# Performance work log

Hardware: AMD Instinct MI355X
Metric: run time of the kernel (lower is better)

## Reference

```python
import jax, jax.numpy as jnp
import numpy as np

V, D, H = 32000, 512, 512
B, T, MAX_LEN = 32, 128, 48


def setup_inputs() -> dict:
    key = jax.random.key(0)
    ks = jax.random.split(key, 12)
    s = 0.02  # xavier-ish scale
    return {
        "inputs": jax.random.randint(ks[0], (B, 1), 0, V),
        "context": jax.random.normal(ks[1], (B, 1, H), dtype=jnp.float32),
        "max_len": MAX_LEN,
        "encoder_outputs": jax.random.normal(ks[2], (B, T, H), dtype=jnp.float32),
        "emb": jax.random.normal(ks[3], (V, D), dtype=jnp.float32) * s,
        "gru_Wih": jax.random.normal(ks[4], (3 * H, D + H), dtype=jnp.float32) * s,
        "gru_Whh": jax.random.normal(ks[5], (3 * H, H), dtype=jnp.float32) * s,
        "gru_bih": jax.random.normal(ks[6], (3 * H,), dtype=jnp.float32) * s,
        "gru_bhh": jax.random.normal(ks[7], (3 * H,), dtype=jnp.float32) * s,
        "lin_W": jax.random.normal(ks[8], (V, 2 * H), dtype=jnp.float32) * s,
        "lin_b": jax.random.normal(ks[9], (V,), dtype=jnp.float32) * s,
        "attn_W": jax.random.normal(ks[10], (H, H), dtype=jnp.float32) * s,
        "attn_b": jax.random.normal(ks[11], (H,), dtype=jnp.float32) * s,
    }


def reference(inputs, context, max_len, encoder_outputs, emb, gru_Wih, gru_Whh,
              gru_bih, gru_bhh, lin_W, lin_b, attn_W, attn_b):
    Bsz, Tlen, Hdim = encoder_outputs.shape
    ctx0 = context[:, 0, :]          # B,H  (last encoder hidden)
    e0 = emb[inputs[:, 0]]           # B,D  (start symbol embedding)
    h0 = jnp.zeros((Bsz, Hdim), dtype=context.dtype)
    # attn linear on encoder outputs is loop-invariant -> hoist
    energies = jnp.einsum('bth,gh->btg', encoder_outputs, attn_W) + attn_b  # B,T,H

    def gru_step(x, h):
        gi = x @ gru_Wih.T + gru_bih
        gh = h @ gru_Whh.T + gru_bhh
        ir, iz, inn = jnp.split(gi, 3, axis=-1)
        hr, hz, hn = jnp.split(gh, 3, axis=-1)
        r = jax.nn.sigmoid(ir + hr)
        z = jax.nn.sigmoid(iz + hz)
        n = jnp.tanh(inn + r * hn)
        return (1.0 - z) * n + z * h

    def step(carry, _):
        h, ctx, e = carry
        h = gru_step(jnp.concatenate([e, ctx], axis=-1), h)
        score = jnp.concatenate([h, ctx], axis=-1) @ lin_W.T + lin_b  # B,V
        logp = jax.nn.log_softmax(score, axis=-1)
        e_next = emb[jnp.argmax(logp, axis=-1)]                       # greedy feedback
        alpha = jax.nn.softmax(jnp.einsum('bth,bh->bt', energies, h), axis=-1)
        ctx_next = jnp.einsum('bt,bth->bh', alpha, encoder_outputs)
        return (h, ctx_next, e_next), logp

    _, logps = jax.lax.scan(step, (h0, ctx0, e0), None, length=max_len)
    # logps: (max_len, B, V) -> cat along dim1 then view => (B*max_len, V)
    return jnp.transpose(logps, (1, 0, 2)).reshape(Bsz * max_len, -1)
```

## Files before the change

### kernel.cpp

```cpp
#include <hip/hip_runtime.h>
#include <hip/hip_bf16.h>

#define V  32000
#define D  512
#define H  512
#define B  32
#define T  128
#define L  48
#define KLIN 1024
#define KGRU 1536

typedef __attribute__((ext_vector_type(8))) short bf16x8;
typedef __attribute__((ext_vector_type(4))) float f32x4;

__device__ __forceinline__ void split1(float f, unsigned short* hi, unsigned short* lo) {
    unsigned u  = __float_as_uint(f);
    unsigned uh = u + (0x7FFFu + ((u >> 16) & 1u));
    unsigned short hs = (unsigned short)(uh >> 16);
    float hf = __uint_as_float(((unsigned)hs) << 16);
    float l  = f - hf;
    unsigned ul = __float_as_uint(l);
    ul += 0x7FFFu + ((ul >> 16) & 1u);
    *hi = hs;
    *lo = (unsigned short)(ul >> 16);
}

__device__ __forceinline__ void split8(const float* __restrict__ p, bf16x8& hi, bf16x8& lo) {
    float4 w0 = reinterpret_cast<const float4*>(p)[0];
    float4 w1 = reinterpret_cast<const float4*>(p)[1];
    float w[8] = {w0.x, w0.y, w0.z, w0.w, w1.x, w1.y, w1.z, w1.w};
    #pragma unroll
    for (int i = 0; i < 8; ++i) {
        unsigned u  = __float_as_uint(w[i]);
        unsigned uh = u + (0x7FFFu + ((u >> 16) & 1u));
        unsigned short hs = (unsigned short)(uh >> 16);
        float hf = __uint_as_float(((unsigned)hs) << 16);
        float l  = w[i] - hf;
        unsigned ul = __float_as_uint(l);
        ul += 0x7FFFu + ((ul >> 16) & 1u);
        hi[i] = (short)hs;
        lo[i] = (short)(ul >> 16);
    }
}

__global__ void presplit_lin(const float* __restrict__ src,
                             unsigned short* __restrict__ hi, unsigned short* __restrict__ lo)
{
    long i = (long)blockIdx.x * 256 + threadIdx.x;
    if (i >= (long)V * KLIN / 8) return;
    bf16x8 h8, l8;
    split8(src + i * 8, h8, l8);
    *(bf16x8*)(hi + i * 8) = h8;
    *(bf16x8*)(lo + i * 8) = l8;
}

__global__ void presplit_gru(const float* __restrict__ Wih, const float* __restrict__ Whh,
                             unsigned short* __restrict__ hi, unsigned short* __restrict__ lo)
{
    int i = blockIdx.x * 256 + threadIdx.x;
    if (i >= 1536 * 192) return;
    int col = i / 192, k = (i % 192) * 8;
    const float* src = (k < 1024) ? (Wih + (size_t)col * 1024 + k)
                                  : (Whh + (size_t)col * 512 + (k - 1024));
    bf16x8 h8, l8;
    split8(src, h8, l8);
    *(bf16x8*)(hi + (size_t)col * KGRU + k) = h8;
    *(bf16x8*)(lo + (size_t)col * KGRU + k) = l8;
}

__global__ void init_state(const int* __restrict__ inputs, const float* __restrict__ context,
                           const float* __restrict__ emb, float* __restrict__ h_t,
                           unsigned short* __restrict__ Xghi, unsigned short* __restrict__ Xglo,
                           unsigned short* __restrict__ Xlhi, unsigned short* __restrict__ Xllo)
{
    int idx = blockIdx.x * 256 + threadIdx.x;
    int b = idx >> 9, j = idx & 511;
    int tok = inputs[b];
    float e = emb[(size_t)tok * D + j];
    split1(e, &Xghi[b * KGRU + j], &Xglo[b * KGRU + j]);
    float c = context[b * H + j];
    split1(c, &Xghi[b * KGRU + 512 + j], &Xglo[b * KGRU + 512 + j]);
    split1(c, &Xlhi[b * KLIN + 512 + j], &Xllo[b * KLIN + 512 + j]);
    Xghi[b * KGRU + 1024 + j] = 0;
    Xglo[b * KGRU + 1024 + j] = 0;
    h_t[j * 32 + b] = 0.f;
}

__global__ void __launch_bounds__(256) energies_gemm(
    const float* __restrict__ enc, const float* __restrict__ attnW,
    const float* __restrict__ attnb, float* __restrict__ energies)
{
    int wave = threadIdx.x >> 6, lane = threadIdx.x & 63;
    int col = blockIdx.y * 64 + wave * 16 + (lane & 15);
    int kg  = (lane >> 4) * 8;
    int arow0 = blockIdx.x * 32 + (lane & 15);
    f32x4 acc0 = {0.f,0.f,0.f,0.f}, acc1 = {0.f,0.f,0.f,0.f};
    for (int k0 = 0; k0 < 512; k0 += 32) {
        bf16x8 bh, bl;  split8(attnW + (size_t)col * 512 + k0 + kg, bh, bl);
        bf16x8 a0h, a0l; split8(enc + (size_t)arow0 * 512 + k0 + kg, a0h, a0l);
        bf16x8 a1h, a1l; split8(enc + (size_t)(arow0 + 16) * 512 + k0 + kg, a1h, a1l);
        acc0 = __builtin_amdgcn_mfma_f32_16x16x32_bf16(a0h, bh, acc0, 0, 0, 0);
        acc1 = __builtin_amdgcn_mfma_f32_16x16x32_bf16(a1h, bh, acc1, 0, 0, 0);
        acc0 = __builtin_amdgcn_mfma_f32_16x16x32_bf16(a0l, bh, acc0, 0, 0, 0);
        acc1 = __builtin_amdgcn_mfma_f32_16x16x32_bf16(a1l, bh, acc1, 0, 0, 0);
        acc0 = __builtin_amdgcn_mfma_f32_16x16x32_bf16(a0h, bl, acc0, 0, 0, 0);
        acc1 = __builtin_amdgcn_mfma_f32_16x16x32_bf16(a1h, bl, acc1, 0, 0, 0);
    }
    float bias = attnb[col];
    int r0 = (lane >> 4) * 4;
    #pragma unroll
    for (int i = 0; i < 4; ++i) {
        int row = blockIdx.x * 32 + r0 + i;
        energies[(size_t)row * 512 + col]        = acc0[i] + bias;
        energies[(size_t)(row + 16) * 512 + col] = acc1[i] + bias;
    }
}

__global__ void __launch_bounds__(384) gru_fused(
    const unsigned short* __restrict__ Ghi, const unsigned short* __restrict__ Glo,
    const unsigned short* __restrict__ Xghi_r, const unsigned short* __restrict__ Xglo_r,
    unsigned short* __restrict__ Xghi_w, unsigned short* __restrict__ Xglo_w,
    unsigned short* __restrict__ Xlhi_w, unsigned short* __restrict__ Xllo_w,
    const float* __restrict__ bih, const float* __restrict__ bhh,
    float* __restrict__ h_t)
{
    __shared__ float AI[3][32][16], AH[3][32][16];
    __shared__ float R[32][16], Z[32][16];
    int w = threadIdx.x >> 6, lane = threadIdx.x & 63;
    int g = (w < 3) ? w : w - 3;
    int half = (w >= 3) ? 1 : 0;
    int c = lane & 15, grp = lane >> 4, kg = grp * 8;
    int j = blockIdx.x * 16 + c;
    int gcol = g * 512 + j;
    const unsigned short* wh = Ghi + (size_t)gcol * KGRU;
    const unsigned short* wl = Glo + (size_t)gcol * KGRU;
    const unsigned short* xh = Xghi_r + (size_t)c * KGRU;
    const unsigned short* xl = Xglo_r + (size_t)c * KGRU;
    f32x4 aI0 = {0.f,0.f,0.f,0.f}, aI1 = {0.f,0.f,0.f,0.f};
    f32x4 aH0 = {0.f,0.f,0.f,0.f}, aH1 = {0.f,0.f,0.f,0.f};
    for (int k0 = half * 512; k0 < half * 512 + 512; k0 += 32) {
        bf16x8 bh = *(const bf16x8*)(wh + k0 + kg);
        bf16x8 bl = *(const bf16x8*)(wl + k0 + kg);
        bf16x8 a0h = *(const bf16x8*)(xh + k0 + kg);
        bf16x8 a0l = *(const bf16x8*)(xl + k0 + kg);
        bf16x8 a1h = *(const bf16x8*)(xh + 16 * KGRU + k0 + kg);
        bf16x8 a1l = *(const bf16x8*)(xl + 16 * KGRU + k0 + kg);
        aI0 = __builtin_amdgcn_mfma_f32_16x16x32_bf16(a0h, bh, aI0, 0, 0, 0);
        aI1 = __builtin_amdgcn_mfma_f32_16x16x32_bf16(a1h, bh, aI1, 0, 0, 0);
        aI0 = __builtin_amdgcn_mfma_f32_16x16x32_bf16(a0l, bh, aI0, 0, 0, 0);
        aI1 = __builtin_amdgcn_mfma_f32_16x16x32_bf16(a1l, bh, aI1, 0, 0, 0);
        aI0 = __builtin_amdgcn_mfma_f32_16x16x32_bf16(a0h, bl, aI0, 0, 0, 0);
        aI1 = __builtin_amdgcn_mfma_f32_16x16x32_bf16(a1h, bl, aI1, 0, 0, 0);
    }
    for (int k0 = 1024 + half * 256; k0 < 1024 + half * 256 + 256; k0 += 32) {
        bf16x8 bh = *(const bf16x8*)(wh + k0 + kg);
        bf16x8 bl = *(const bf16x8*)(wl + k0 + kg);
        bf16x8 a0h = *(const bf16x8*)(xh + k0 + kg);
        bf16x8 a0l = *(const bf16x8*)(xl + k0 + kg);
        bf16x8 a1h = *(const bf16x8*)(xh + 16 * KGRU + k0 + kg);
        bf16x8 a1l = *(const bf16x8*)(xl + 16 * KGRU + k0 + kg);
        aH0 = __builtin_amdgcn_mfma_f32_16x16x32_bf16(a0h, bh, aH0, 0, 0, 0);
        aH1 = __builtin_amdgcn_mfma_f32_16x16x32_bf16(a1h, bh, aH1, 0, 0, 0);
        aH0 = __builtin_amdgcn_mfma_f32_16x16x32_bf16(a0l, bh, aH0, 0, 0, 0);
        aH1 = __builtin_amdgcn_mfma_f32_16x16x32_bf16(a1l, bh, aH1, 0, 0, 0);
        aH0 = __builtin_amdgcn_mfma_f32_16x16x32_bf16(a0h, bl, aH0, 0, 0, 0);
        aH1 = __builtin_amdgcn_mfma_f32_16x16x32_bf16(a1h, bl, aH1, 0, 0, 0);
    }
    if (w >= 3) {
        #pragma unroll
        for (int i = 0; i < 4; ++i) {
            AI[g][grp * 4 + i][c] = aI0[i];  AI[g][grp * 4 + i + 16][c] = aI1[i];
            AH[g][grp * 4 + i][c] = aH0[i];  AH[g][grp * 4 + i + 16][c] = aH1[i];
        }
    }
    __syncthreads();
    float gi[8], gh[8];
    if (w < 3) {
        float bi = bih[gcol], bhv = bhh[gcol];
        #pragma unroll
        for (int i = 0; i < 4; ++i) {
            gi[i]     = aI0[i] + AI[g][grp * 4 + i][c]      + bi;
            gi[i + 4] = aI1[i] + AI[g][grp * 4 + i + 16][c] + bi;
            gh[i]     = aH0[i] + AH[g][grp * 4 + i][c]      + bhv;
            gh[i + 4] = aH1[i] + AH[g][grp * 4 + i + 16][c] + bhv;
        }
        if (w == 0) {
            #pragma unroll
            for (int i = 0; i < 8; ++i) {
                int b = (i < 4) ? grp * 4 + i : grp * 4 + (i - 4) + 16;
                R[b][c] = 1.f / (1.f + expf(-(gi[i] + gh[i])));
            }
        } else if (w == 1) {
            #pragma unroll
            for (int i = 0; i < 8; ++i) {
                int b = (i < 4) ? grp * 4 + i : grp * 4 + (i - 4) + 16;
                Z[b][c] = 1.f / (1.f + expf(-(gi[i] + gh[i])));
            }
        }
    }
    __syncthreads();
    if (w == 2) {
        float4 h0 = *(const float4*)(h_t + (size_t)j * 32 + grp * 4);
        float4 h1 = *(const float4*)(h_t + (size_t)j * 32 + grp * 4 + 16);
        float hold[8] = {h0.x, h0.y, h0.z, h0.w, h1.x, h1.y, h1.z, h1.w};
        float hn[8];
        #pragma unroll
        for (int i = 0; i < 8; ++i) {
            int b = (i < 4) ? grp * 4 + i : grp * 4 + (i - 4) + 16;
            float n = tanhf(gi[i] + R[b][c] * gh[i]);
            float z = Z[b][c];
            hn[i] = (1.f - z) * n + z * hold[i];
        }
        *(float4*)(h_t + (size_t)j * 32 + grp * 4)      = make_float4(hn[0], hn[1], hn[2], hn[3]);
        *(float4*)(h_t + (size_t)j * 32 + grp * 4 + 16) = make_float4(hn[4], hn[5], hn[6], hn[7]);
        #pragma unroll
        for (int i = 0; i < 8; ++i) {
            int b = (i < 4) ? grp * 4 + i : grp * 4 + (i - 4) + 16;
            split1(hn[i], &Xlhi_w[(size_t)b * KLIN + j], &Xllo_w[(size_t)b * KLIN + j]);
            split1(hn[i], &Xghi_w[(size_t)b * KGRU + 1024 + j], &Xglo_w[(size_t)b * KGRU + 1024 + j]);
        }
    }
}

template<bool PS>
__global__ void __launch_bounds__(256) score_attn(
    const float* __restrict__ linW,
    const unsigned short* __restrict__ Whi, const unsigned short* __restrict__ Wlo,
    const float* __restrict__ linb,
    const unsigned short* __restrict__ Xlhi_r, const unsigned short* __restrict__ Xllo_r,
    unsigned short* __restrict__ Xlhi_w, unsigned short* __restrict__ Xllo_w,
    unsigned short* __restrict__ Xghi_w, unsigned short* __restrict__ Xglo_w,
    const float* __restrict__ h_t, const float* __restrict__ energies,
    const float* __restrict__ enc,
    float* __restrict__ out, float* __restrict__ Pm, float* __restrict__ Ps,
    int* __restrict__ Pa, int t)
{
    __shared__ float Lm[4][32], Ls[4][32];
    __shared__ int   La[4][32];
    __shared__ float hrow[512], aw[128], red[256];
    int tid = threadIdx.x;
    if (blockIdx.x < 500) {
        int wave = tid >> 6, lane = tid & 63;
        int c = lane & 15, grp = lane >> 4, kg = grp * 8;
        int col = blockIdx.x * 64 + wave * 16 + c;
        const unsigned short* x0h = Xlhi_r + (size_t)c * KLIN + kg;
        const unsigned short* x0l = Xllo_r + (size_t)c * KLIN + kg;
        f32x4 acc0 = {0.f,0.f,0.f,0.f}, acc1 = {0.f,0.f,0.f,0.f};
        #pragma unroll 2
        for (int k0 = 0; k0 < 1024; k0 += 32) {
            bf16x8 bh, bl;
            if (PS) {
                bh = *(const bf16x8*)(Whi + (size_t)col * 1024 + k0 + kg);
                bl = *(const bf16x8*)(Wlo + (size_t)col * 1024 + k0 + kg);
            } else {
                split8(linW + (size_t)col * 1024 + k0 + kg, bh, bl);
            }
            bf16x8 a0h = *(const bf16x8*)(x0h + k0);
            bf16x8 a0l = *(const bf16x8*)(x0l + k0);
            bf16x8 a1h = *(const bf16x8*)(x0h + 16 * KLIN + k0);
            bf16x8 a1l = *(const bf16x8*)(x0l + 16 * KLIN + k0);
            acc0 = __builtin_amdgcn_mfma_f32_16x16x32_bf16(a0h, bh, acc0, 0, 0, 0);
            acc1 = __builtin_amdgcn_mfma_f32_16x16x32_bf16(a1h, bh, acc1, 0, 0, 0);
            acc0 = __builtin_amdgcn_mfma_f32_16x16x32_bf16(a0l, bh, acc0, 0, 0, 0);
            acc1 = __builtin_amdgcn_mfma_f32_16x16x32_bf16(a1l, bh, acc1, 0, 0, 0);
            acc0 = __builtin_amdgcn_mfma_f32_16x16x32_bf16(a0h, bl, acc0, 0, 0, 0);
            acc1 = __builtin_amdgcn_mfma_f32_16x16x32_bf16(a1h, bl, acc1, 0, 0, 0);
        }
        float bias = linb[col];
        float v[8];
        int r0 = grp * 4;
        #pragma unroll
        for (int i = 0; i < 4; ++i) {
            v[i]     = acc0[i] + bias;
            v[i + 4] = acc1[i] + bias;
            out[(size_t)((r0 + i) * L + t) * V + col]      = v[i];
            out[(size_t)((r0 + i + 16) * L + t) * V + col] = v[i + 4];
        }
        #pragma unroll
        for (int i = 0; i < 8; ++i) {
            float m = v[i]; int mc = col;
            #pragma unroll
            for (int d = 1; d < 16; d <<= 1) {
                float om = __shfl_xor(m, d); int oc = __shfl_xor(mc, d);
                if (om > m || (om == m && oc < mc)) { m = om; mc = oc; }
            }
            float s = expf(v[i] - m);
            #pragma unroll
            for (int d = 1; d < 16; d <<= 1) s += __shfl_xor(s, d);
            if (c == 0) {
                int row = (i < 4) ? r0 + i : r0 + (i - 4) + 16;
                Lm[wave][row] = m; La[wave][row] = mc; Ls[wave][row] = s;
            }
        }
        __syncthreads();
        if (tid < 32) {
            float M = Lm[0][tid]; int a = La[0][tid];
            #pragma unroll
            for (int q = 1; q < 4; ++q) {
                float om = Lm[q][tid]; int oa = La[q][tid];
                if (om > M || (om == M && oa < a)) { M = om; a = oa; }
            }
            float S = 0.f;
            #pragma unroll
            for (int q = 0; q < 4; ++q) S += Ls[q][tid] * expf(Lm[q][tid] - M);
            Pm[tid * 500 + blockIdx.x] = M;
            Pa[tid * 500 + blockIdx.x] = a;
            Ps[tid * 500 + blockIdx.x] = S;
        }
    } else {
        int b = blockIdx.x - 500;
        for (int j = tid; j < 512; j += 256) hrow[j] = h_t[(size_t)j * 32 + b];
        __syncthreads();
        {
            int tt = tid >> 1, half = tid & 1;
            const float4* e4 = (const float4*)(energies + ((size_t)(b * T + tt)) * 512 + half * 256);
            const float4* h4 = (const float4*)(hrow + half * 256);
            float p = 0.f;
            #pragma unroll 4
            for (int k = 0; k < 64; ++k) {
                float4 a = e4[k], cc = h4[k];
                p += a.x * cc.x + a.y * cc.y + a.z * cc.z + a.w * cc.w;
            }
            p += __shfl_xor(p, 1);
            if (half == 0) aw[tt] = p;
        }
        __syncthreads();
        red[tid] = (tid < 128) ? aw[tid] : -INFINITY; __syncthreads();
        for (int s = 128; s > 0; s >>= 1) { if (tid < s) red[tid] = fmaxf(red[tid], red[tid + s]); __syncthreads(); }
        float am = red[0];
        __syncthreads();
        if (tid < 128) { float e = expf(aw[tid] - am); aw[tid] = e; red[tid] = e; } else red[tid] = 0.f;
        __syncthreads();
        for (int s = 128; s > 0; s >>= 1) { if (tid < s) red[tid] += red[tid + s]; __syncthreads(); }
        float asum = red[0];
        __syncthreads();
        float c0 = 0.f, c1 = 0.f;
        for (int tt2 = 0; tt2 < T; ++tt2) {
            float a = aw[tt2];
            const float* er = enc + ((size_t)(b * T + tt2)) * 512;
            c0 += a * er[tid];
            c1 += a * er[tid + 256];
        }
        c0 /= asum; c1 /= asum;
        split1(c0, &Xlhi_w[(size_t)b * KLIN + 512 + tid],       &Xllo_w[(size_t)b * KLIN + 512 + tid]);
        split1(c1, &Xlhi_w[(size_t)b * KLIN + 512 + tid + 256], &Xllo_w[(size_t)b * KLIN + 512 + tid + 256]);
        split1(c0, &Xghi_w[(size_t)b * KGRU + 512 + tid],       &Xglo_w[(size_t)b * KGRU + 512 + tid]);
        split1(c1, &Xghi_w[(size_t)b * KGRU + 512 + tid + 256], &Xglo_w[(size_t)b * KGRU + 512 + tid + 256]);
    }
}

__global__ void __launch_bounds__(256) finalize(
    const float* __restrict__ Pm, const float* __restrict__ Ps, const int* __restrict__ Pa,
    const float* __restrict__ emb,
    unsigned short* __restrict__ Xghi_w, unsigned short* __restrict__ Xglo_w,
    float* __restrict__ lse_buf, int t)
{
    __shared__ float sm[256]; __shared__ int sa[256]; __shared__ float ss[256];
    int b = blockIdx.x, tid = threadIdx.x;
    float m1 = -INFINITY, s1 = 0.f; int a1 = 0x7fffffff;
    float m2 = -INFINITY, s2 = 0.f; int a2 = 0x7fffffff;
    if (tid < 500)       { m1 = Pm[b * 500 + tid];       a1 = Pa[b * 500 + tid];       s1 = Ps[b * 500 + tid]; }
    if (tid + 256 < 500) { m2 = Pm[b * 500 + tid + 256]; a2 = Pa[b * 500 + tid + 256]; s2 = Ps[b * 500 + tid + 256]; }
    float m = m1; int a = a1;
    if (m2 > m || (m2 == m && a2 < a)) { m = m2; a = a2; }
    sm[tid] = m; sa[tid] = a; __syncthreads();
    for (int s = 128; s > 0; s >>= 1) {
        if (tid < s) {
            float om = sm[tid + s]; int oa = sa[tid + s];
            if (om > sm[tid] || (om == sm[tid] && oa < sa[tid])) { sm[tid] = om; sa[tid] = oa; }
        }
        __syncthreads();
    }
    float M = sm[0]; int amax = sa[0];
    __syncthreads();
    float sc = s1 * expf(m1 - M) + s2 * expf(m2 - M);
    ss[tid] = sc; __syncthreads();
    for (int s = 128; s > 0; s >>= 1) { if (tid < s) ss[tid] += ss[tid + s]; __syncthreads(); }
    if (tid == 0) lse_buf[b * L + t] = M + logf(ss[0]);
    for (int j = tid; j < 512; j += 256)
        split1(emb[(size_t)amax * D + j], &Xghi_w[(size_t)b * KGRU + j], &Xglo_w[(size_t)b * KGRU + j]);
}

__global__ void __launch_bounds__(256) subtract_lse(float* __restrict__ out,
                                                    const float* __restrict__ lse_buf)
{
    long i4 = (long)blockIdx.x * 256 + threadIdx.x;
    int row = (int)(i4 / 8000);
    float l = lse_buf[row];
    float4* p = (float4*)out + i4;
    float4 v = *p;
    v.x -= l; v.y -= l; v.z -= l; v.w -= l;
    *p = v;
}

extern "C" void kernel_launch(void* const* d_in, const int* in_sizes, int n_in,
                              void* d_out, int out_size, void* d_ws, size_t ws_size,
                              hipStream_t stream) {
    const int*   inputs  = (const int*)d_in[0];
    const float* context = (const float*)d_in[1];
    const float* enc     = (const float*)d_in[3];
    const float* emb     = (const float*)d_in[4];
    const float* Wih     = (const float*)d_in[5];
    const float* Whh     = (const float*)d_in[6];
    const float* bih     = (const float*)d_in[7];
    const float* bhh     = (const float*)d_in[8];
    const float* linW    = (const float*)d_in[9];
    const float* linb    = (const float*)d_in[10];
    const float* attnW   = (const float*)d_in[11];
    const float* attnb   = (const float*)d_in[12];
    float* out = (float*)d_out;

    char* w = (char*)d_ws;
    unsigned short* Ghi = (unsigned short*)w; w += (size_t)1536 * KGRU * 2;
    unsigned short* Glo = (unsigned short*)w; w += (size_t)1536 * KGRU * 2;
    float* energies = (float*)w;              w += (size_t)B * T * 512 * 4;
    float* h_t      = (float*)w;              w += (size_t)H * B * 4;
    unsigned short* Xghi[2]; unsigned short* Xglo[2];
    unsigned short* Xlhi[2]; unsigned short* Xllo[2];
    for (int q = 0; q < 2; ++q) {
        Xghi[q] = (unsigned short*)w; w += (size_t)B * KGRU * 2;
        Xglo[q] = (unsigned short*)w; w += (size_t)B * KGRU * 2;
        Xlhi[q] = (unsigned short*)w; w += (size_t)B * KLIN * 2;
        Xllo[q] = (unsigned short*)w; w += (size_t)B * KLIN * 2;
    }
    float* Pm = (float*)w; w += (size_t)32 * 500 * 4;
    float* Ps = (float*)w; w += (size_t)32 * 500 * 4;
    int*   Pa = (int*)w;   w += (size_t)32 * 500 * 4;
    float* lse_buf = (float*)w; w += (size_t)B * L * 4;
    size_t base_need = (size_t)(w - (char*)d_ws);
    unsigned short* Whi = (unsigned short*)w; w += (size_t)V * KLIN * 2;
    unsigned short* Wlo = (unsigned short*)w; w += (size_t)V * KLIN * 2;
    bool pres = ws_size >= base_need + (size_t)V * KLIN * 4;

    if (pres)
        presplit_lin<<<16000, 256, 0, stream>>>(linW, Whi, Wlo);
    presplit_gru<<<1152, 256, 0, stream>>>(Wih, Whh, Ghi, Glo);
    init_state<<<64, 256, 0, stream>>>(inputs, context, emb, h_t, Xghi[0], Xglo[0], Xlhi[0], Xllo[0]);
    energies_gemm<<<dim3(128, 8), 256, 0, stream>>>(enc, attnW, attnb, energies);

    for (int t = 0; t < L; ++t) {
        int r = t & 1, n = (t + 1) & 1;
        gru_fused<<<32, 384, 0, stream>>>(Ghi, Glo, Xghi[r], Xglo[r],
                                          Xghi[n], Xglo[n], Xlhi[r], Xllo[r],
                                          bih, bhh, h_t);
        if (pres)
            score_attn<true><<<532, 256, 0, stream>>>(linW, Whi, Wlo, linb,
                Xlhi[r], Xllo[r], Xlhi[n], Xllo[n], Xghi[n], Xglo[n],
                h_t, energies, enc, out, Pm, Ps, Pa, t);
        else
            score_attn<false><<<532, 256, 0, stream>>>(linW, Whi, Wlo, linb,
                Xlhi[r], Xllo[r], Xlhi[n], Xllo[n], Xghi[n], Xglo[n],
                h_t, energies, enc, out, Pm, Ps, Pa, t);
        finalize<<<32, 256, 0, stream>>>(Pm, Ps, Pa, emb, Xghi[n], Xglo[n], lse_buf, t);
    }
    subtract_lse<<<48000, 256, 0, stream>>>(out, lse_buf);
}
```

Baseline: 4.637 ms.

## Quantize vocab projection to scaled FP8 MFMA with exact argmax rescue

Replaces the split-bf16 vocab projection (hi/lo weights, three MFMAs per tile) with a pre-scaled FP8 e4m3 copy of lin_W in an MFMA-friendly tiled layout. Each step then streams a quarter of the weight bytes and issues one FP8 MFMA per tile. To keep the greedy feedback path correct, the per-block reduction now tracks the top two candidates. The finalize kernel recomputes in fp32 every column whose approximate score lies within a fixed delta of the maximum and takes the exact argmax from those. The risks are lower accuracy in the emitted log-probabilities and extra finalize work whenever many candidates fall inside the rescue window.

```diff
diff --git a/kernel.cpp b/kernel.cpp
--- a/kernel.cpp
+++ b/kernel.cpp
@@ -1,5 +1,6 @@
 #include <hip/hip_runtime.h>
 #include <hip/hip_bf16.h>
+#include <hip/hip_fp8.h>
 
 #define V  32000
 #define D  512
@@ -9,6 +10,7 @@
 #define L  48
 #define KLIN 1024
 #define KGRU 1536
+#define RESCUE_DELTA 0.16f
 
 typedef __attribute__((ext_vector_type(8))) short bf16x8;
 typedef __attribute__((ext_vector_type(4))) float f32x4;
@@ -43,15 +45,38 @@
     }
 }
 
-__global__ void presplit_lin(const float* __restrict__ src,
-                             unsigned short* __restrict__ hi, unsigned short* __restrict__ lo)
+__device__ __forceinline__ unsigned char to_fp8(float v) {
+    __hip_fp8_e4m3 q(v);
+    return (unsigned char)q.__x;
+}
+
+__device__ __forceinline__ void merge2(float& m1, int& i1, float& m2, int& i2,
+                                       float om1, int oi1, float om2, int oi2) {
+    bool ogt = (om1 > m1) || (om1 == m1 && oi1 < i1);
+    float t1 = ogt ? om1 : m1; int ti1 = ogt ? oi1 : i1;
+    float l1 = ogt ? m1 : om1; int li1 = ogt ? i1 : oi1;
+    float w2 = ogt ? om2 : m2; int wi2 = ogt ? oi2 : i2;
+    bool lgt = (l1 > w2) || (l1 == w2 && li1 < wi2);
+    m1 = t1; i1 = ti1;
+    m2 = lgt ? l1 : w2; i2 = lgt ? li1 : wi2;
+}
+
+__global__ void presplit_lin8(const float* __restrict__ src, unsigned char* __restrict__ W8)
 {
     long i = (long)blockIdx.x * 256 + threadIdx.x;
-    if (i >= (long)V * KLIN / 8) return;
-    bf16x8 h8, l8;
-    split8(src + i * 8, h8, l8);
-    *(bf16x8*)(hi + i * 8) = h8;
-    *(bf16x8*)(lo + i * 8) = l8;
+    if (i >= (long)V * 128) return;
+    int col = (int)(i >> 7), k = (int)(i & 127) << 3;
+    const float* p = src + (size_t)col * 1024 + k;
+    float4 w0 = reinterpret_cast<const float4*>(p)[0];
+    float4 w1 = reinterpret_cast<const float4*>(p)[1];
+    float w[8] = {w0.x, w0.y, w0.z, w0.w, w1.x, w1.y, w1.z, w1.w};
+    unsigned long long pk = 0;
+    #pragma unroll
+    for (int j = 0; j < 8; ++j)
+        pk |= ((unsigned long long)to_fp8(w[j] * 1024.f)) << (8 * j);
+    size_t addr = (size_t)(col >> 4) * 16384 + (size_t)(k >> 5) * 512
+                + (size_t)((k >> 3) & 3) * 128 + (size_t)(col & 15) * 8;
+    *(unsigned long long*)(W8 + addr) = pk;
 }
 
 __global__ void presplit_gru(const float* __restrict__ Wih, const float* __restrict__ Whh,
@@ -71,7 +96,7 @@
 __global__ void init_state(const int* __restrict__ inputs, const float* __restrict__ context,
                            const float* __restrict__ emb, float* __restrict__ h_t,
                            unsigned short* __restrict__ Xghi, unsigned short* __restrict__ Xglo,
-                           unsigned short* __restrict__ Xlhi, unsigned short* __restrict__ Xllo)
+                           unsigned char* __restrict__ X8, float* __restrict__ Xf)
 {
     int idx = blockIdx.x * 256 + threadIdx.x;
     int b = idx >> 9, j = idx & 511;
@@ -80,9 +105,10 @@
     split1(e, &Xghi[b * KGRU + j], &Xglo[b * KGRU + j]);
     float c = context[b * H + j];
     split1(c, &Xghi[b * KGRU + 512 + j], &Xglo[b * KGRU + 512 + j]);
-    split1(c, &Xlhi[b * KLIN + 512 + j], &Xllo[b * KLIN + 512 + j]);
     Xghi[b * KGRU + 1024 + j] = 0;
     Xglo[b * KGRU + 1024 + j] = 0;
+    X8[b * 1024 + 512 + j] = to_fp8(c * 64.f);
+    Xf[b * 1024 + 512 + j] = c;
     h_t[j * 32 + b] = 0.f;
 }
 
@@ -120,7 +146,7 @@
     const unsigned short* __restrict__ Ghi, const unsigned short* __restrict__ Glo,
     const unsigned short* __restrict__ Xghi_r, const unsigned short* __restrict__ Xglo_r,
     unsigned short* __restrict__ Xghi_w, unsigned short* __restrict__ Xglo_w,
-    unsigned short* __restrict__ Xlhi_w, unsigned short* __restrict__ Xllo_w,
+    unsigned char* __restrict__ X8_w, float* __restrict__ Xf_w,
     const float* __restrict__ bih, const float* __restrict__ bhh,
     float* __restrict__ h_t)
 {
@@ -216,96 +242,89 @@
         #pragma unroll
         for (int i = 0; i < 8; ++i) {
             int b = (i < 4) ? grp * 4 + i : grp * 4 + (i - 4) + 16;
-            split1(hn[i], &Xlhi_w[(size_t)b * KLIN + j], &Xllo_w[(size_t)b * KLIN + j]);
+            X8_w[(size_t)b * 1024 + j] = to_fp8(hn[i] * 64.f);
+            Xf_w[(size_t)b * 1024 + j] = hn[i];
             split1(hn[i], &Xghi_w[(size_t)b * KGRU + 1024 + j], &Xglo_w[(size_t)b * KGRU + 1024 + j]);
         }
     }
 }
 
-template<bool PS>
 __global__ void __launch_bounds__(256) score_attn(
-    const float* __restrict__ linW,
-    const unsigned short* __restrict__ Whi, const unsigned short* __restrict__ Wlo,
-    const float* __restrict__ linb,
-    const unsigned short* __restrict__ Xlhi_r, const unsigned short* __restrict__ Xllo_r,
-    unsigned short* __restrict__ Xlhi_w, unsigned short* __restrict__ Xllo_w,
+    const unsigned char* __restrict__ W8, const float* __restrict__ linb,
+    const unsigned char* __restrict__ X8_r,
+    unsigned char* __restrict__ X8_w, float* __restrict__ Xf_w,
     unsigned short* __restrict__ Xghi_w, unsigned short* __restrict__ Xglo_w,
     const float* __restrict__ h_t, const float* __restrict__ energies,
     const float* __restrict__ enc,
-    float* __restrict__ out, float* __restrict__ Pm, float* __restrict__ Ps,
-    int* __restrict__ Pa, int t)
-{
-    __shared__ float Lm[4][32], Ls[4][32];
-    __shared__ int   La[4][32];
+    float* __restrict__ out,
+    float* __restrict__ Pm, int* __restrict__ Pa,
+    float* __restrict__ Pm2, int* __restrict__ Pa2,
+    float* __restrict__ Ps, int t)
+{
+    __shared__ float Lm1[4][32], Lm2[4][32], Ls[4][32];
+    __shared__ int   Li1[4][32], Li2[4][32];
     __shared__ float hrow[512], aw[128], red[256];
     int tid = threadIdx.x;
     if (blockIdx.x < 500) {
         int wave = tid >> 6, lane = tid & 63;
-        int c = lane & 15, grp = lane >> 4, kg = grp * 8;
+        int c = lane & 15, grp = lane >> 4;
         int col = blockIdx.x * 64 + wave * 16 + c;
-        const unsigned short* x0h = Xlhi_r + (size_t)c * KLIN + kg;
-        const unsigned short* x0l = Xllo_r + (size_t)c * KLIN + kg;
+        const unsigned char* wp = W8 + (size_t)(blockIdx.x * 4 + wave) * 16384 + grp * 128 + c * 8;
+        const unsigned char* x0 = X8_r + (size_t)c * 1024 + grp * 8;
+        const unsigned char* x1 = x0 + 16 * 1024;
         f32x4 acc0 = {0.f,0.f,0.f,0.f}, acc1 = {0.f,0.f,0.f,0.f};
-        #pragma unroll 2
-        for (int k0 = 0; k0 < 1024; k0 += 32) {
-            bf16x8 bh, bl;
-            if (PS) {
-                bh = *(const bf16x8*)(Whi + (size_t)col * 1024 + k0 + kg);
-                bl = *(const bf16x8*)(Wlo + (size_t)col * 1024 + k0 + kg);
-            } else {
-                split8(linW + (size_t)col * 1024 + k0 + kg, bh, bl);
-            }
-            bf16x8 a0h = *(const bf16x8*)(x0h + k0);
-            bf16x8 a0l = *(const bf16x8*)(x0l + k0);
-            bf16x8 a1h = *(const bf16x8*)(x0h + 16 * KLIN + k0);
-            bf16x8 a1l = *(const bf16x8*)(x0l + 16 * KLIN + k0);
-            acc0 = __builtin_amdgcn_mfma_f32_16x16x32_bf16(a0h, bh, acc0, 0, 0, 0);
-            acc1 = __builtin_amdgcn_mfma_f32_16x16x32_bf16(a1h, bh, acc1, 0, 0, 0);
-            acc0 = __builtin_amdgcn_mfma_f32_16x16x32_bf16(a0l, bh, acc0, 0, 0, 0);
-            acc1 = __builtin_amdgcn_mfma_f32_16x16x32_bf16(a1l, bh, acc1, 0, 0, 0);
-            acc0 = __builtin_amdgcn_mfma_f32_16x16x32_bf16(a0h, bl, acc0, 0, 0, 0);
-            acc1 = __builtin_amdgcn_mfma_f32_16x16x32_bf16(a1h, bl, acc1, 0, 0, 0);
+        #pragma unroll 4
+        for (int kb = 0; kb < 32; ++kb) {
+            long wb = *(const long*)(wp + kb * 512);
+            long a0 = *(const long*)(x0 + kb * 32);
+            long a1 = *(const long*)(x1 + kb * 32);
+            acc0 = __builtin_amdgcn_mfma_f32_16x16x32_fp8_fp8(a0, wb, acc0, 0, 0, 0);
+            acc1 = __builtin_amdgcn_mfma_f32_16x16x32_fp8_fp8(a1, wb, acc1, 0, 0, 0);
         }
         float bias = linb[col];
         float v[8];
         int r0 = grp * 4;
         #pragma unroll
         for (int i = 0; i < 4; ++i) {
-            v[i]     = acc0[i] + bias;
-            v[i + 4] = acc1[i] + bias;
+            v[i]     = acc0[i] * (1.f / 65536.f) + bias;
+            v[i + 4] = acc1[i] * (1.f / 65536.f) + bias;
             out[(size_t)((r0 + i) * L + t) * V + col]      = v[i];
             out[(size_t)((r0 + i + 16) * L + t) * V + col] = v[i + 4];
         }
         #pragma unroll
         for (int i = 0; i < 8; ++i) {
-            float m = v[i]; int mc = col;
+            float m1 = v[i]; int i1 = col; float m2 = -INFINITY; int i2 = 0x7fffffff;
             #pragma unroll
             for (int d = 1; d < 16; d <<= 1) {
-                float om = __shfl_xor(m, d); int oc = __shfl_xor(mc, d);
-                if (om > m || (om == m && oc < mc)) { m = om; mc = oc; }
+                float om1 = __shfl_xor(m1, d); int oi1 = __shfl_xor(i1, d);
+                float om2 = __shfl_xor(m2, d); int oi2 = __shfl_xor(i2, d);
+                merge2(m1, i1, m2, i2, om1, oi1, om2, oi2);
             }
-            float s = expf(v[i] - m);
+            float s = expf(v[i] - m1);
             #pragma unroll
             for (int d = 1; d < 16; d <<= 1) s += __shfl_xor(s, d);
             if (c == 0) {
                 int row = (i < 4) ? r0 + i : r0 + (i - 4) + 16;
-                Lm[wave][row] = m; La[wave][row] = mc; Ls[wave][row] = s;
+                Lm1[wave][row] = m1; Li1[wave][row] = i1;
+                Lm2[wave][row] = m2; Li2[wave][row] = i2;
+                Ls[wave][row] = s;
             }
         }
         __syncthreads();
         if (tid < 32) {
-            float M = Lm[0][tid]; int a = La[0][tid];
+            float m1 = Lm1[0][tid]; int i1 = Li1[0][tid];
+            float m2 = Lm2[0][tid]; int i2 = Li2[0][tid];
             #pragma unroll
-            for (int q = 1; q < 4; ++q) {
-                float om = Lm[q][tid]; int oa = La[q][tid];
-                if (om > M || (om == M && oa < a)) { M = om; a = oa; }
-            }
+            for (int q = 1; q < 4; ++q)
+                merge2(m1, i1, m2, i2, Lm1[q][tid], Li1[q][tid], Lm2[q][tid], Li2[q][tid]);
             float S = 0.f;
             #pragma unroll
-            for (int q = 0; q < 4; ++q) S += Ls[q][tid] * expf(Lm[q][tid] - M);
-            Pm[tid * 500 + blockIdx.x] = M;
-            Pa[tid * 500 + blockIdx.x] = a;
-            Ps[tid * 500 + blockIdx.x] = S;
+            for (int q = 0; q < 4; ++q) S += Ls[q][tid] * expf(Lm1[q][tid] - m1);
+            Pm [tid * 500 + blockIdx.x] = m1;
+            Pa [tid * 500 + blockIdx.x] = i1;
+            Pm2[tid * 500 + blockIdx.x] = m2;
+            Pa2[tid * 500 + blockIdx.x] = i2;
+            Ps [tid * 500 + blockIdx.x] = S;
         }
     } else {
         int b = blockIdx.x - 500;
@@ -342,41 +361,88 @@
             c1 += a * er[tid + 256];
         }
         c0 /= asum; c1 /= asum;
-        split1(c0, &Xlhi_w[(size_t)b * KLIN + 512 + tid],       &Xllo_w[(size_t)b * KLIN + 512 + tid]);
-        split1(c1, &Xlhi_w[(size_t)b * KLIN + 512 + tid + 256], &Xllo_w[(size_t)b * KLIN + 512 + tid + 256]);
+        X8_w[(size_t)b * 1024 + 512 + tid]       = to_fp8(c0 * 64.f);
+        X8_w[(size_t)b * 1024 + 512 + tid + 256] = to_fp8(c1 * 64.f);
+        Xf_w[(size_t)b * 1024 + 512 + tid]       = c0;
+        Xf_w[(size_t)b * 1024 + 512 + tid + 256] = c1;
         split1(c0, &Xghi_w[(size_t)b * KGRU + 512 + tid],       &Xglo_w[(size_t)b * KGRU + 512 + tid]);
         split1(c1, &Xghi_w[(size_t)b * KGRU + 512 + tid + 256], &Xglo_w[(size_t)b * KGRU + 512 + tid + 256]);
     }
 }
 
 __global__ void __launch_bounds__(256) finalize(
-    const float* __restrict__ Pm, const float* __restrict__ Ps, const int* __restrict__ Pa,
-    const float* __restrict__ emb,
+    const float* __restrict__ Pm, const int* __restrict__ Pa,
+    const float* __restrict__ Pm2, const int* __restrict__ Pa2,
+    const float* __restrict__ Ps,
+    const float* __restrict__ linW, const float* __restrict__ linb,
+    const float* __restrict__ Xf_r, const float* __restrict__ emb,
     unsigned short* __restrict__ Xghi_w, unsigned short* __restrict__ Xglo_w,
     float* __restrict__ lse_buf, int t)
 {
-    __shared__ float sm[256]; __shared__ int sa[256]; __shared__ float ss[256];
+    __shared__ float xb[1024];
+    __shared__ float sred[256];
+    __shared__ int   sidx[256];
+    __shared__ int   list[256];
+    __shared__ float cscore[256];
+    __shared__ int   ncand_sh;
     int b = blockIdx.x, tid = threadIdx.x;
-    float m1 = -INFINITY, s1 = 0.f; int a1 = 0x7fffffff;
-    float m2 = -INFINITY, s2 = 0.f; int a2 = 0x7fffffff;
-    if (tid < 500)       { m1 = Pm[b * 500 + tid];       a1 = Pa[b * 500 + tid];       s1 = Ps[b * 500 + tid]; }
-    if (tid + 256 < 500) { m2 = Pm[b * 500 + tid + 256]; a2 = Pa[b * 500 + tid + 256]; s2 = Ps[b * 500 + tid + 256]; }
-    float m = m1; int a = a1;
-    if (m2 > m || (m2 == m && a2 < a)) { m = m2; a = a2; }
-    sm[tid] = m; sa[tid] = a; __syncthreads();
+    for (int j = tid; j < 1024; j += 256) xb[j] = Xf_r[(size_t)b * 1024 + j];
+    if (tid == 0) ncand_sh = 0;
+    float m = -INFINITY;
+    for (int i = tid; i < 500; i += 256) m = fmaxf(m, Pm[b * 500 + i]);
+    sred[tid] = m; __syncthreads();
+    for (int s = 128; s > 0; s >>= 1) { if (tid < s) sred[tid] = fmaxf(sred[tid], sred[tid + s]); __syncthreads(); }
+    float M = sred[0];
+    float thresh = M - RESCUE_DELTA;
+    __syncthreads();
+    float S = 0.f;
+    for (int i = tid; i < 500; i += 256) {
+        float pm = Pm[b * 500 + i];
+        S += Ps[b * 500 + i] * expf(pm - M);
+        if (pm >= thresh) {
+            int p = atomicAdd(&ncand_sh, 1);
+            if (p < 256) list[p] = Pa[b * 500 + i];
+        }
+        if (Pm2[b * 500 + i] >= thresh) {
+            int p = atomicAdd(&ncand_sh, 64);
+            for (int q = 0; q < 64; ++q) if (p + q < 256) list[p + q] = i * 64 + q;
+        }
+    }
+    sred[tid] = S; __syncthreads();
+    for (int s = 128; s > 0; s >>= 1) { if (tid < s) sred[tid] += sred[tid + s]; __syncthreads(); }
+    if (tid == 0) lse_buf[b * L + t] = M + logf(sred[0]);
+    __syncthreads();
+    int nc = ncand_sh < 256 ? ncand_sh : 256;
+    int wv = tid >> 6, lane = tid & 63;
+    for (int ci = wv; ci < nc; ci += 4) {
+        int col = list[ci];
+        const float* wr = linW + (size_t)col * 1024 + lane * 16;
+        const float* xr = xb + lane * 16;
+        float s = 0.f;
+        #pragma unroll
+        for (int j = 0; j < 16; j += 4) {
+            float4 a = *(const float4*)(wr + j);
+            s += a.x * xr[j] + a.y * xr[j + 1] + a.z * xr[j + 2] + a.w * xr[j + 3];
+        }
+        #pragma unroll
+        for (int d = 1; d < 64; d <<= 1) s += __shfl_xor(s, d);
+        if (lane == 0) cscore[ci] = s + linb[col];
+    }
+    __syncthreads();
+    float bm = -INFINITY; int bi = 0x7fffffff;
+    for (int ci = tid; ci < nc; ci += 256) {
+        float vv = cscore[ci]; int cc = list[ci];
+        if (vv > bm || (vv == bm && cc < bi)) { bm = vv; bi = cc; }
+    }
+    sred[tid] = bm; sidx[tid] = bi; __syncthreads();
     for (int s = 128; s > 0; s >>= 1) {
         if (tid < s) {
-            float om = sm[tid + s]; int oa = sa[tid + s];
-            if (om > sm[tid] || (om == sm[tid] && oa < sa[tid])) { sm[tid] = om; sa[tid] = oa; }
-        }
-        __syncthreads();
-    }
-    float M = sm[0]; int amax = sa[0];
-    __syncthreads();
-    float sc = s1 * expf(m1 - M) + s2 * expf(m2 - M);
-    ss[tid] = sc; __syncthreads();
-    for (int s = 128; s > 0; s >>= 1) { if (tid < s) ss[tid] += ss[tid + s]; __syncthreads(); }
-    if (tid == 0) lse_buf[b * L + t] = M + logf(ss[0]);
+            float ov = sred[tid + s]; int oi = sidx[tid + s];
+            if (ov > sred[tid] || (ov == sred[tid] && oi < sidx[tid])) { sred[tid] = ov; sidx[tid] = oi; }
+        }
+        __syncthreads();
+    }
+    int amax = sidx[0];
     for (int j = tid; j < 512; j += 256)
         split1(emb[(size_t)amax * D + j], &Xghi_w[(size_t)b * KGRU + j], &Xglo_w[(size_t)b * KGRU + j]);
 }
@@ -416,42 +482,37 @@
     float* energies = (float*)w;              w += (size_t)B * T * 512 * 4;
     float* h_t      = (float*)w;              w += (size_t)H * B * 4;
     unsigned short* Xghi[2]; unsigned short* Xglo[2];
-    unsigned short* Xlhi[2]; unsigned short* Xllo[2];
+    unsigned char* X8[2]; float* Xf[2];
     for (int q = 0; q < 2; ++q) {
         Xghi[q] = (unsigned short*)w; w += (size_t)B * KGRU * 2;
         Xglo[q] = (unsigned short*)w; w += (size_t)B * KGRU * 2;
-        Xlhi[q] = (unsigned short*)w; w += (size_t)B * KLIN * 2;
-        Xllo[q] = (unsigned short*)w; w += (size_t)B * KLIN * 2;
-    }
-    float* Pm = (float*)w; w += (size_t)32 * 500 * 4;
-    float* Ps = (float*)w; w += (size_t)32 * 500 * 4;
-    int*   Pa = (int*)w;   w += (size_t)32 * 500 * 4;
+        Xf[q]   = (float*)w;          w += (size_t)B * KLIN * 4;
+        X8[q]   = (unsigned char*)w;  w += (size_t)B * KLIN;
+    }
+    float* Pm  = (float*)w; w += (size_t)32 * 500 * 4;
+    int*   Pa  = (int*)w;   w += (size_t)32 * 500 * 4;
+    float* Pm2 = (float*)w; w += (size_t)32 * 500 * 4;
+    int*   Pa2 = (int*)w;   w += (size_t)32 * 500 * 4;
+    float* Ps  = (float*)w; w += (size_t)32 * 500 * 4;
     float* lse_buf = (float*)w; w += (size_t)B * L * 4;
-    size_t base_need = (size_t)(w - (char*)d_ws);
-    unsigned short* Whi = (unsigned short*)w; w += (size_t)V * KLIN * 2;
-    unsigned short* Wlo = (unsigned short*)w; w += (size_t)V * KLIN * 2;
-    bool pres = ws_size >= base_need + (size_t)V * KLIN * 4;
-
-    if (pres)
-        presplit_lin<<<16000, 256, 0, stream>>>(linW, Whi, Wlo);
+    unsigned char* W8 = (unsigned char*)w; w += (size_t)V * KLIN;
+
+    presplit_lin8<<<16000, 256, 0, stream>>>(linW, W8);
     presplit_gru<<<1152, 256, 0, stream>>>(Wih, Whh, Ghi, Glo);
-    init_state<<<64, 256, 0, stream>>>(inputs, context, emb, h_t, Xghi[0], Xglo[0], Xlhi[0], Xllo[0]);
+    init_state<<<64, 256, 0, stream>>>(inputs, context, emb, h_t, Xghi[0], Xglo[0], X8[0], Xf[0]);
     energies_gemm<<<dim3(128, 8), 256, 0, stream>>>(enc, attnW, attnb, energies);
 
     for (int t = 0; t < L; ++t) {
         int r = t & 1, n = (t + 1) & 1;
         gru_fused<<<32, 384, 0, stream>>>(Ghi, Glo, Xghi[r], Xglo[r],
-                                          Xghi[n], Xglo[n], Xlhi[r], Xllo[r],
+                                          Xghi[n], Xglo[n], X8[r], Xf[r],
                                           bih, bhh, h_t);
-        if (pres)
-            score_attn<true><<<532, 256, 0, stream>>>(linW, Whi, Wlo, linb,
-                Xlhi[r], Xllo[r], Xlhi[n], Xllo[n], Xghi[n], Xglo[n],
-                h_t, energies, enc, out, Pm, Ps, Pa, t);
-        else
-            score_attn<false><<<532, 256, 0, stream>>>(linW, Whi, Wlo, linb,
-                Xlhi[r], Xllo[r], Xlhi[n], Xllo[n], Xghi[n], Xglo[n],
-                h_t, energies, enc, out, Pm, Ps, Pa, t);
-        finalize<<<32, 256, 0, stream>>>(Pm, Ps, Pa, emb, Xghi[n], Xglo[n], lse_buf, t);
+        score_attn<<<532, 256, 0, stream>>>(W8, linb, X8[r],
+                                            X8[n], Xf[n], Xghi[n], Xglo[n],
+                                            h_t, energies, enc, out,
+                                            Pm, Pa, Pm2, Pa2, Ps, t);
+        finalize<<<32, 256, 0, stream>>>(Pm, Pa, Pm2, Pa2, Ps, linW, linb,
+                                         Xf[r], emb, Xghi[n], Xglo[n], lse_buf, t);
     }
     subtract_lse<<<48000, 256, 0, stream>>>(out, lse_buf);
 }
```

Measured after the change: 6.333 ms. +36.6%, slower.
